# Performance work log

Measured on AMD Instinct MI355X. Metric: run time of the kernel, lower is better.

The kernel has to match this reference:

```python
import jax, jax.numpy as jnp
import numpy as np

T = 131072      # timesteps
F = 8           # features per timestep; close price at column 3
HIDDEN = 256
MAX_K = 10
BUF = 50        # sliding buffer size


def _hfd_all(p):
    """Higuchi fractal dimension over a trailing window of BUF prices, for every t.

    Replicates: buffer grows to BUF then slides; HFD computed only once
    len(buffer) > MAX_K, else 0. p: [T] float.
    """
    Tn = p.shape[0]
    t = jnp.arange(Tn)
    n = jnp.minimum(t + 1, BUF)                 # buffer length at step t
    nm1 = n - 1
    nm1f = nm1.astype(p.dtype)
    starts = jnp.maximum(0, t + 1 - BUF)
    idx = jnp.clip(starts[:, None] + jnp.arange(BUF)[None, :], 0, Tn - 1)
    W = p[idx]                                   # [T, BUF] left-aligned windows

    lk_cols = []
    for k in range(1, MAX_K + 1):
        # lag-k abs diffs within each window: D[t, q] = |W[t, q+k] - W[t, q]|
        D = jnp.abs(W[:, k:] - W[:, :-k])        # [T, BUF-k]
        pos = jnp.arange(BUF - k)
        D = jnp.where(pos[None, :] + k <= nm1[:, None], D, jnp.zeros((), p.dtype))
        acc = jnp.zeros(Tn, p.dtype)
        for m in range(k):
            pm = np.arange(m, BUF - k, k)        # positions m, m+k, ... in D
            S = D[:, pm].sum(axis=1)             # sum of |arr[m+(j+1)k]-arr[m+jk]|
            length = jnp.where(nm1 >= m, (nm1 - m) // k + 1, 0)  # len(idxs)
            good = length >= 2
            lf = jnp.maximum(length, 1).astype(p.dtype)
            acc = acc + jnp.where(good, S * nm1f / (lf * k), jnp.zeros((), p.dtype))
        lk_cols.append(acc / k)
    Lk = jnp.stack(lk_cols, axis=1)              # [T, MAX_K]

    # log-log linear fit (polyfit deg 1) over k with Lk > 0
    logk = jnp.log(jnp.arange(1, MAX_K + 1, dtype=p.dtype))
    valid = Lk > 0
    wv = valid.astype(p.dtype)
    loglk = jnp.where(valid, jnp.log(jnp.where(valid, Lk, jnp.ones((), p.dtype))), jnp.zeros((), p.dtype))
    c = wv.sum(1)
    sx = (wv * logk).sum(1)
    sy = loglk.sum(1)
    sxy = (loglk * logk).sum(1)
    sxx = (wv * logk * logk).sum(1)
    denom = c * sxx - sx * sx
    safe = jnp.where(denom != 0, denom, jnp.ones((), p.dtype))
    slope = (c * sxy - sx * sy) / safe
    hfd = -slope
    return jnp.where((c > 1) & (n >= MAX_K + 1), hfd, jnp.zeros((), p.dtype))


def setup_inputs() -> dict:
    key = jax.random.key(0)
    k1, k2, k3 = jax.random.split(key, 3)
    x = jax.random.normal(k1, (T, F), jnp.float32)
    w_lin = jax.random.normal(k2, (HIDDEN, 1), jnp.float32) * 0.1   # nn.Linear(1, hidden)
    b_lin = jax.random.normal(k3, (HIDDEN,), jnp.float32) * 0.1
    return {"x": x, "w_lin": w_lin, "b_lin": b_lin}


def reference(x, w_lin, b_lin):
    hfd = _hfd_all(x[:, 3])                      # [T]
    # relu(linear(hfd[:, None])) with in_features=1
    return jax.nn.relu(hfd[:, None] * w_lin[:, 0][None, :] + b_lin[None, :])
```

## Files before the change

kernel.cpp:

```cpp
#include <hip/hip_runtime.h>
#include <math.h>

#define T_TOTAL 131072
#define FEAT    8
#define HIDDEN  256
#define MAXK    10
#define BUF     50
#define BT      256

__device__ __forceinline__ float fit_loglog(const float Lk[MAXK]) {
    const float logk[MAXK] = {0.0f,        0.6931472f, 1.0986123f, 1.3862944f,
                              1.6094379f,  1.7917595f, 1.9459101f, 2.0794415f,
                              2.1972246f,  2.3025851f};
    float c = 0.f, sx = 0.f, sy = 0.f, sxy = 0.f, sxx = 0.f;
#pragma unroll
    for (int i = 0; i < MAXK; ++i) {
        if (Lk[i] > 0.0f) {
            const float lx = logk[i];
            const float ly = logf(Lk[i]);
            c   += 1.0f;
            sx  += lx;
            sy  += ly;
            sxy += ly * lx;
            sxx += lx * lx;
        }
    }
    float denom = c * sxx - sx * sx;
    denom = (denom != 0.0f) ? denom : 1.0f;
    const float slope = (c * sxy - sx * sy) / denom;
    return (c > 1.0f) ? -slope : 0.0f;
}

__global__ __launch_bounds__(BT) void hfd_fused(const float* __restrict__ x,
                                                const float* __restrict__ w_lin,
                                                const float* __restrict__ b_lin,
                                                float4* __restrict__ outv) {
    __shared__ float sp[BT / 64][128];

    const int tid   = threadIdx.x;
    const int lane  = tid & 63;
    const int wid   = tid >> 6;
    const int wbase = blockIdx.x * BT + (wid << 6);
    float* wsp = sp[wid];

    {
        const int gt0 = wbase - (BUF - 1) + lane;
        wsp[lane] = (gt0 >= 0) ? x[(size_t)gt0 * FEAT + 3] : 0.0f;
        if (lane < 49) {
            const int gt1 = gt0 + 64;
            wsp[64 + lane] = (gt1 >= 0) ? x[(size_t)gt1 * FEAT + 3] : 0.0f;
        }
    }

    const int t = wbase + lane;
    float hfd = 0.0f;

    if (t >= BUF - 1) {
        float w[BUF];
#pragma unroll
        for (int q = 0; q < BUF; ++q) w[q] = wsp[lane + q];

        float Lk[MAXK];
#pragma unroll
        for (int k = 1; k <= MAXK; ++k) {
            float acc = 0.0f;
#pragma unroll
            for (int m = 0; m < k; ++m) {
                float S = 0.0f;
#pragma unroll
                for (int q = m; q + k <= BUF - 1; q += k)
                    S += fabsf(w[q + k] - w[q]);
                const int len = (BUF - 1 - m) / k + 1;
                acc += S * ((float)(BUF - 1) / (float)(len * k));
            }
            Lk[k - 1] = acc / (float)k;
        }
        hfd = fit_loglog(Lk);
    } else if (t >= MAXK) {
        const int   nm1  = t;
        const float nm1f = (float)nm1;
        const float* wp  = &wsp[BUF - 1];

        float Lk[MAXK];
        for (int k = 1; k <= MAXK; ++k) {
            float acc = 0.0f;
            for (int m = 0; m < k; ++m) {
                float S = 0.0f;
                for (int q = m; q + k <= nm1; q += k)
                    S += fabsf(wp[q + k] - wp[q]);
                const int length = (nm1 >= m) ? ((nm1 - m) / k + 1) : 0;
                if (length >= 2)
                    acc += S * nm1f / (float)(length * k);
            }
            Lk[k - 1] = acc / (float)k;
        }
        hfd = fit_loglog(Lk);
    }

    const float4 wv = ((const float4*)w_lin)[lane];
    const float4 bv = ((const float4*)b_lin)[lane];

#pragma unroll 16
    for (int r = 0; r < 64; ++r) {
        const float h = __shfl(hfd, r, 64);
        float4 o;
        o.x = fmaxf(fmaf(h, wv.x, bv.x), 0.0f);
        o.y = fmaxf(fmaf(h, wv.y, bv.y), 0.0f);
        o.z = fmaxf(fmaf(h, wv.z, bv.z), 0.0f);
        o.w = fmaxf(fmaf(h, wv.w, bv.w), 0.0f);
        outv[(size_t)(wbase + r) * (HIDDEN / 4) + lane] = o;
    }
}

extern "C" void kernel_launch(void* const* d_in, const int* in_sizes, int n_in,
                              void* d_out, int out_size, void* d_ws, size_t ws_size,
                              hipStream_t stream) {
    const float* x     = (const float*)d_in[0];
    const float* w_lin = (const float*)d_in[1];
    const float* b_lin = (const float*)d_in[2];
    float4* outv = (float4*)d_out;

    hfd_fused<<<dim3(T_TOTAL / BT), dim3(BT), 0, stream>>>(x, w_lin, b_lin, outv);
}
```

Measured before the change: 146.6 us.

## Compute HFD in one wave per block and spread output stores over four waves

Each block now covers 64 rows instead of 256. A single wavefront computes the 64 HFD values and shares them through LDS. After a barrier, all four wavefronts write the 64x256 output tile, so the store-bound epilogue is spread across more waves. Launch bounds request higher occupancy. The trade-off is that three of the four waves sit idle during the compute phase, and the grid has four times as many blocks.

Measured after the change: 142.0 us. 1.03x faster.

```diff
diff --git a/kernel.cpp b/kernel.cpp
--- a/kernel.cpp
+++ b/kernel.cpp
@@ -6,7 +6,8 @@
 #define HIDDEN  256
 #define MAXK    10
 #define BUF     50
-#define BT      256
+#define RPB     64
+#define NT      256
 
 __device__ __forceinline__ float fit_loglog(const float Lk[MAXK]) {
     const float logk[MAXK] = {0.0f,        0.6931472f, 1.0986123f, 1.3862944f,
@@ -31,84 +32,91 @@
     return (c > 1.0f) ? -slope : 0.0f;
 }
 
-__global__ __launch_bounds__(BT) void hfd_fused(const float* __restrict__ x,
-                                                const float* __restrict__ w_lin,
-                                                const float* __restrict__ b_lin,
-                                                float4* __restrict__ outv) {
-    __shared__ float sp[BT / 64][128];
+__global__ __launch_bounds__(NT, 4) void hfd_fused(const float* __restrict__ x,
+                                                   const float* __restrict__ w_lin,
+                                                   const float* __restrict__ b_lin,
+                                                   float4* __restrict__ outv) {
+    __shared__ float sp[128];
+    __shared__ float shfd[RPB];
 
     const int tid   = threadIdx.x;
     const int lane  = tid & 63;
     const int wid   = tid >> 6;
-    const int wbase = blockIdx.x * BT + (wid << 6);
-    float* wsp = sp[wid];
-
-    {
-        const int gt0 = wbase - (BUF - 1) + lane;
-        wsp[lane] = (gt0 >= 0) ? x[(size_t)gt0 * FEAT + 3] : 0.0f;
-        if (lane < 49) {
-            const int gt1 = gt0 + 64;
-            wsp[64 + lane] = (gt1 >= 0) ? x[(size_t)gt1 * FEAT + 3] : 0.0f;
-        }
-    }
-
-    const int t = wbase + lane;
-    float hfd = 0.0f;
-
-    if (t >= BUF - 1) {
-        float w[BUF];
-#pragma unroll
-        for (int q = 0; q < BUF; ++q) w[q] = wsp[lane + q];
-
-        float Lk[MAXK];
-#pragma unroll
-        for (int k = 1; k <= MAXK; ++k) {
-            float acc = 0.0f;
-#pragma unroll
-            for (int m = 0; m < k; ++m) {
-                float S = 0.0f;
-#pragma unroll
-                for (int q = m; q + k <= BUF - 1; q += k)
-                    S += fabsf(w[q + k] - w[q]);
-                const int len = (BUF - 1 - m) / k + 1;
-                acc += S * ((float)(BUF - 1) / (float)(len * k));
-            }
-            Lk[k - 1] = acc / (float)k;
-        }
-        hfd = fit_loglog(Lk);
-    } else if (t >= MAXK) {
-        const int   nm1  = t;
-        const float nm1f = (float)nm1;
-        const float* wp  = &wsp[BUF - 1];
-
-        float Lk[MAXK];
-        for (int k = 1; k <= MAXK; ++k) {
-            float acc = 0.0f;
-            for (int m = 0; m < k; ++m) {
-                float S = 0.0f;
-                for (int q = m; q + k <= nm1; q += k)
-                    S += fabsf(wp[q + k] - wp[q]);
-                const int length = (nm1 >= m) ? ((nm1 - m) / k + 1) : 0;
-                if (length >= 2)
-                    acc += S * nm1f / (float)(length * k);
-            }
-            Lk[k - 1] = acc / (float)k;
-        }
-        hfd = fit_loglog(Lk);
-    }
+    const int wbase = blockIdx.x * RPB;
 
     const float4 wv = ((const float4*)w_lin)[lane];
     const float4 bv = ((const float4*)b_lin)[lane];
 
-#pragma unroll 16
-    for (int r = 0; r < 64; ++r) {
-        const float h = __shfl(hfd, r, 64);
+    if (wid == 0) {
+        const int gt0 = wbase - (BUF - 1) + lane;
+        sp[lane] = (gt0 >= 0) ? x[(size_t)gt0 * FEAT + 3] : 0.0f;
+        if (lane < BUF - 1) {
+            sp[64 + lane] = x[(size_t)(gt0 + 64) * FEAT + 3];
+        }
+
+        const int t = wbase + lane;
+        float hfd = 0.0f;
+
+        if (t >= BUF - 1) {
+            float w[BUF];
+#pragma unroll
+            for (int q = 0; q < BUF; ++q) w[q] = sp[lane + q];
+
+            float Lk[MAXK];
+#pragma unroll
+            for (int k = 1; k <= MAXK; ++k) {
+                float acc = 0.0f;
+#pragma unroll
+                for (int m = 0; m < k; ++m) {
+                    float S = 0.0f;
+#pragma unroll
+                    for (int q = m; q + k <= BUF - 1; q += k)
+                        S += fabsf(w[q + k] - w[q]);
+                    const int len = (BUF - 1 - m) / k + 1;
+                    acc += S * ((float)(BUF - 1) / (float)(len * k));
+                }
+                Lk[k - 1] = acc / (float)k;
+            }
+            hfd = fit_loglog(Lk);
+        } else if (t >= MAXK) {
+            const int   nm1  = t;
+            const float nm1f = (float)nm1;
+            const float* wp  = &sp[BUF - 1];
+
+            float Lk[MAXK];
+            for (int k = 1; k <= MAXK; ++k) {
+                float acc = 0.0f;
+                for (int m = 0; m < k; ++m) {
+                    float S = 0.0f;
+                    for (int q = m; q + k <= nm1; q += k)
+                        S += fabsf(wp[q + k] - wp[q]);
+                    const int length = (nm1 >= m) ? ((nm1 - m) / k + 1) : 0;
+                    if (length >= 2)
+                        acc += S * nm1f / (float)(length * k);
+                }
+                Lk[k - 1] = acc / (float)k;
+            }
+            hfd = fit_loglog(Lk);
+        }
+
+        shfd[lane] = hfd;
+    }
+
+    __syncthreads();
+
+    float hv[16];
+#pragma unroll
+    for (int it = 0; it < 16; ++it) hv[it] = shfd[(it << 2) + wid];
+
+#pragma unroll
+    for (int it = 0; it < 16; ++it) {
+        const float h = hv[it];
         float4 o;
         o.x = fmaxf(fmaf(h, wv.x, bv.x), 0.0f);
         o.y = fmaxf(fmaf(h, wv.y, bv.y), 0.0f);
         o.z = fmaxf(fmaf(h, wv.z, bv.z), 0.0f);
         o.w = fmaxf(fmaf(h, wv.w, bv.w), 0.0f);
-        outv[(size_t)(wbase + r) * (HIDDEN / 4) + lane] = o;
+        outv[(size_t)(wbase + (it << 2) + wid) * (HIDDEN / 4) + lane] = o;
     }
 }
 
@@ -120,5 +128,5 @@
     const float* b_lin = (const float*)d_in[2];
     float4* outv = (float4*)d_out;
 
-    hfd_fused<<<dim3(T_TOTAL / BT), dim3(BT), 0, stream>>>(x, w_lin, b_lin, outv);
+    hfd_fused<<<dim3(T_TOTAL / RPB), dim3(NT), 0, stream>>>(x, w_lin, b_lin, outv);
 }
```
